# Kernel optimization log

Measured on AMD Instinct MI355X. Metric: run time of the kernel, lower is better.

Reference implementation:

```python
import jax, jax.numpy as jnp
import numpy as np

# Irrep layout: blocks of (multiplicity, l); identical for input and output.
LS = [0, 1, 2, 3]
MULS = [64, 64, 64, 64]
N = 65536
DIM = sum(m * (2 * l + 1) for m, l in zip(MULS, LS))  # 1024
NPATH = len(LS) * len(LS)  # 16 valid (l_out, l_in) paths
MAXM = max(LS)             # max |m| over all paths
NW = sum(mo * mi for mo in MULS for mi in MULS)  # 65536 path weights


def _split_blocks(x):
    """Split flat irrep vector into per-block [n, mul, 2l+1] views."""
    blocks, off = [], 0
    for mul, l in zip(MULS, LS):
        d = mul * (2 * l + 1)
        blocks.append(x[:, off:off + d].reshape(x.shape[0], mul, 2 * l + 1))
        off += d
    return blocks


def setup_inputs() -> dict:
    key = jax.random.key(0)
    k = jax.random.split(key, 5)
    return {
        "x": jax.random.normal(k[0], (N, DIM), jnp.float32),
        "weights": jax.random.normal(k[1], (NW,), jnp.float32) * 0.1,
        "hzero": jax.random.normal(k[2], (NPATH,), jnp.float32),
        "hpos": jax.random.normal(k[3], (NPATH, MAXM), jnp.float32),
        "hneg": jax.random.normal(k[4], (NPATH, MAXM), jnp.float32),
    }


def reference(x, weights, hzero, hpos, hneg):
    xb = _split_blocks(x)
    n = x.shape[0]
    outb = [jnp.zeros((n, mul, 2 * l + 1), x.dtype) for mul, l in zip(MULS, LS)]
    p, off = 0, 0
    for oi, (mo, lo) in enumerate(zip(MULS, LS)):
        for ii, (mi, li) in enumerate(zip(MULS, LS)):
            W = weights[off:off + mo * mi].reshape(mo, mi)
            off += mo * mi
            xi = xb[ii]  # [n, mi, 2*li+1]
            # m = 0 component
            y0 = jnp.einsum('nm,om->no', xi[:, :, li], W) * hzero[p]
            outb[oi] = outb[oi].at[:, :, lo].add(y0)
            # |m| >= 1: O(2)-reduced pos/neg mixing with Wigner-derived couplings
            for m in range(1, min(lo, li) + 1):
                hp, hn = hpos[p, m - 1], hneg[p, m - 1]
                xp, xn = xi[:, :, li + m], xi[:, :, li - m]
                outb[oi] = outb[oi].at[:, :, lo + m].add(
                    jnp.einsum('nm,om->no', hp * xp + hn * xn, W))
                outb[oi] = outb[oi].at[:, :, lo - m].add(
                    jnp.einsum('nm,om->no', hp * xn - hn * xp, W))
            p += 1
    return jnp.concatenate([b.reshape(n, -1) for b in outb], axis=1)
```

## Files before the change

### kernel.cpp

```cpp
#include <hip/hip_runtime.h>


typedef __attribute__((ext_vector_type(8))) short bhalf8_t;
typedef __attribute__((ext_vector_type(4))) float f32x4_t;

#define NROWS 65536
#define DIMV  1024
#define NT    1024
#define RPW   64

#define M0_OFF 0
#define M1_OFF 65536
#define M2_OFF 212992
#define M3_OFF 278528
#define M_TOTAL 294912

#define OP 1028

__device__ __forceinline__ constexpr int xoff(int L) {
    return (L == 0) ? 0 : (L == 1) ? 4608 : (L == 2) ? 18432 : 41472;
}

__device__ __forceinline__ short f2bf(float f) {
    unsigned u = __builtin_bit_cast(unsigned, f);
    u = (u + 0x7FFFu + ((u >> 16) & 1u)) >> 16;
    return (short)u;
}

__global__ __launch_bounds__(256) void build_M(const float* __restrict__ w,
                                               const float* __restrict__ hz,
                                               const float* __restrict__ hp,
                                               const float* __restrict__ hn,
                                               short* __restrict__ M) {
    int idx = blockIdx.x * 256 + threadIdx.x;
    if (idx >= M_TOTAL) return;

    int m, A, B;
    if (idx < M1_OFF)      { m = 0; int lo = idx;            A = lo / 256u; B = lo - A * 256; }
    else if (idx < M2_OFF) { m = 1; int lo = idx - M1_OFF;   A = lo / 384u; B = lo - A * 384; }
    else if (idx < M3_OFF) { m = 2; int lo = idx - M2_OFF;   A = lo / 256u; B = lo - A * 256; }
    else                   { m = 3; int lo = idx - M3_OFF;   A = lo / 128u; B = lo - A * 128; }

    int ob, so, o, ib, si, i;
    if (m == 0) { ob = A >> 6;       so = 0;            o = A & 63;
                  ib = B >> 6;       si = 0;            i = B & 63; }
    else        { ob = (A >> 7) + m; so = (A >> 6) & 1; o = A & 63;
                  ib = (B >> 7) + m; si = (B >> 6) & 1; i = B & 63; }

    int p = ob * 4 + ib;
    float wv = w[p * 4096 + o * 64 + i];
    float coef;
    if (m == 0) {
        coef = hz[p];
    } else {
        float hpv = hp[p * 3 + (m - 1)];
        float hnv = hn[p * 3 + (m - 1)];
        coef = (so == 0) ? ((si == 0) ? hpv : hnv)
                         : ((si == 0) ? -hnv : hpv);
    }
    M[idx] = f2bf(wv * coef);
}

template<int L>
__device__ __forceinline__ void stage_block(const float* __restrict__ x, int rowbase,
                                            short* __restrict__ xb, int tid) {
    constexpr int nch = 2 * L + 1;
    constexpr int d4  = 16 * nch;
    constexpr int RS  = nch * 72;
    constexpr int bo  = 64 * L * L;
#pragma unroll
    for (int e = 0; e < nch; ++e) {
        int id  = e * NT + tid;
        int row = id / d4;
        int cc  = id - row * d4;
        int col = cc * 4;
        const float4 v = *(const float4*)(x + (size_t)(rowbase + row) * DIMV + bo + col);
        short* dst = &xb[row * RS];
        { int ci = col;     int i = ci / nch; int ji = ci - i * nch; dst[ji * 72 + i] = f2bf(v.x); }
        { int ci = col + 1; int i = ci / nch; int ji = ci - i * nch; dst[ji * 72 + i] = f2bf(v.y); }
        { int ci = col + 2; int i = ci / nch; int ji = ci - i * nch; dst[ji * 72 + i] = f2bf(v.z); }
        { int ci = col + 3; int i = ci / nch; int ji = ci - i * nch; dst[ji * 72 + i] = f2bf(v.w); }
    }
}

template<int L>
__device__ __forceinline__ void compute_block(const short* __restrict__ xb,
                                              const short* __restrict__ Mg,
                                              int m, int Wm, int cb, int lr, int q,
                                              f32x4_t (&acc)[4][4]) {
    if (m > L) return;
    constexpr int nch = 2 * L + 1;
    constexpr int RS  = nch * 72;
    const int nsi = (m == 0) ? 1 : 2;
    for (int si = 0; si < nsi; ++si) {
        const int ji    = L + ((si == 0) ? m : -m);
        const int kbase = (m == 0) ? (L << 6) : (((L - m) << 7) + (si << 6));
#pragma unroll
        for (int kk = 0; kk < 2; ++kk) {
            bhalf8_t a[4];
            const int eo = ji * 72 + kk * 32 + q * 8;
#pragma unroll
            for (int r = 0; r < 4; ++r)
                a[r] = *(const bhalf8_t*)&xb[(r * 16 + lr) * RS + eo];
            const int ko = kbase + kk * 32 + q * 8;
#pragma unroll
            for (int c = 0; c < 4; ++c) {
                const bhalf8_t b = *(const bhalf8_t*)&Mg[(cb + c * 16 + lr) * Wm + ko];
#pragma unroll
                for (int r = 0; r < 4; ++r)
                    acc[c][r] = __builtin_amdgcn_mfma_f32_16x16x32_bf16(
                        a[r], b, acc[c][r], 0, 0, 0);
            }
        }
    }
}

__global__ __launch_bounds__(NT) void tp_main(const float* __restrict__ x,
                                              const short* __restrict__ Mall,
                                              float* __restrict__ out) {
    __shared__ __align__(16) char smem[147456];
    short* __restrict__ xbuf = (short*)smem;
    float* __restrict__ obuf = (float*)smem;

    const int tid  = threadIdx.x;
    const int lane = tid & 63;
    const int lr   = lane & 15;
    const int q    = lane >> 4;
    const int wv   = tid >> 6;
    const int rowbase = blockIdx.x * RPW;

    int m, cb;
    if (wv < 4)       { m = 0; cb = wv << 6; }
    else if (wv < 10) { m = 1; cb = (wv - 4) << 6; }
    else if (wv < 14) { m = 2; cb = (wv - 10) << 6; }
    else              { m = 3; cb = (wv - 14) << 6; }
    const int Wm   = (m == 1) ? 384 : ((m == 3) ? 128 : 256);
    const int Moff = (m == 0) ? M0_OFF : (m == 1) ? M1_OFF : (m == 2) ? M2_OFF : M3_OFF;
    const short* __restrict__ Mg = Mall + Moff;

    f32x4_t acc[4][4];
#pragma unroll
    for (int c = 0; c < 4; ++c)
#pragma unroll
        for (int r = 0; r < 4; ++r)
            acc[c][r] = (f32x4_t){0.f, 0.f, 0.f, 0.f};

    stage_block<0>(x, rowbase, xbuf + xoff(0), tid);
    stage_block<1>(x, rowbase, xbuf + xoff(1), tid);
    stage_block<2>(x, rowbase, xbuf + xoff(2), tid);
    stage_block<3>(x, rowbase, xbuf + xoff(3), tid);
    __syncthreads();

    compute_block<0>(xbuf + xoff(0), Mg, m, Wm, cb, lr, q, acc);
    compute_block<1>(xbuf + xoff(1), Mg, m, Wm, cb, lr, q, acc);
    compute_block<2>(xbuf + xoff(2), Mg, m, Wm, cb, lr, q, acc);
    compute_block<3>(xbuf + xoff(3), Mg, m, Wm, cb, lr, q, acc);

    int origc[4];
#pragma unroll
    for (int c = 0; c < 4; ++c) {
        const int P = cb + c * 16 + lr;
        int ob, o, jo;
        if (m == 0) { ob = P >> 6;       o = P & 63; jo = ob; }
        else        { ob = (P >> 7) + m; o = P & 63;
                      jo = ob + ((((P >> 6) & 1) == 0) ? m : -m); }
        origc[c] = 64 * ob * ob + o * (2 * ob + 1) + jo;
    }

#pragma unroll
    for (int r = 0; r < 4; ++r) {
        __syncthreads();
#pragma unroll
        for (int c = 0; c < 4; ++c) {
#pragma unroll
            for (int g = 0; g < 4; ++g)
                obuf[(q * 4 + g) * OP + origc[c]] = acc[c][r][g];
        }
        __syncthreads();
#pragma unroll
        for (int it = 0; it < 4; ++it) {
            const int j   = it * NT + tid;
            const int row = j >> 8;
            const int c4  = (j & 255) << 2;
            const float4 v = *(const float4*)&obuf[row * OP + c4];
            *(float4*)&out[(size_t)(rowbase + r * 16 + row) * DIMV + c4] = v;
        }
    }
}

extern "C" void kernel_launch(void* const* d_in, const int* in_sizes, int n_in,
                              void* d_out, int out_size, void* d_ws, size_t ws_size,
                              hipStream_t stream) {
    const float* x   = (const float*)d_in[0];
    const float* wts = (const float*)d_in[1];
    const float* hz  = (const float*)d_in[2];
    const float* hp  = (const float*)d_in[3];
    const float* hn  = (const float*)d_in[4];
    float* out = (float*)d_out;
    short* M   = (short*)d_ws;

    build_M<<<dim3(M_TOTAL / 256), dim3(256), 0, stream>>>(wts, hz, hp, hn, M);
    tp_main<<<dim3(NROWS / RPW), dim3(NT), 0, stream>>>(x, M, out);
}
```

Baseline: 528.7 us.

## Split x permutation into separate kernel and stream GEMM operands from global

Adds a pre-pass kernel that converts x to bf16 and writes it into per-m contiguous K-major segments in workspace. The main GEMM kernel then reads A and B fragments directly from global memory, with no LDS staging of x, and uses only a small LDS buffer for the output transpose, which should allow higher occupancy. A fallback kernel with reduced LDS, staging one L-block at a time, is used when the workspace is too small. The cost is an extra global round trip for the permuted bf16 x, about 128 MB written and read back.

```diff
diff --git a/kernel.cpp b/kernel.cpp
--- a/kernel.cpp
+++ b/kernel.cpp
@@ -6,8 +6,6 @@
 
 #define NROWS 65536
 #define DIMV  1024
-#define NT    1024
-#define RPW   64
 
 #define M0_OFF 0
 #define M1_OFF 65536
@@ -15,11 +13,14 @@
 #define M3_OFF 278528
 #define M_TOTAL 294912
 
+#define XG_SH_OFF 524288
+#define SEG0 0
+#define SEG1 16777216
+#define SEG2 41943040
+#define SEG3 58720256
+#define WS_NEED 135266304ull
+
 #define OP 1028
-
-__device__ __forceinline__ constexpr int xoff(int L) {
-    return (L == 0) ? 0 : (L == 1) ? 4608 : (L == 2) ? 18432 : 41472;
-}
 
 __device__ __forceinline__ short f2bf(float f) {
     unsigned u = __builtin_bit_cast(unsigned, f);
@@ -61,16 +62,145 @@
     M[idx] = f2bf(wv * coef);
 }
 
+__global__ __launch_bounds__(256) void permute_x(const float* __restrict__ x,
+                                                 short* __restrict__ xg) {
+    __shared__ __align__(16) short lbuf[16 * 1024];
+    const int t = threadIdx.x;
+    const int rowbase = blockIdx.x << 4;
+
+#pragma unroll
+    for (int p = 0; p < 16; ++p) {
+        const int id  = p * 256 + t;
+        const int row = id >> 8;
+        const int c4  = id & 255;
+        const float4 v = *(const float4*)(x + (size_t)(rowbase + row) * DIMV + c4 * 4);
+        short* d = &lbuf[row * 1024 + c4 * 4];
+        d[0] = f2bf(v.x); d[1] = f2bf(v.y); d[2] = f2bf(v.z); d[3] = f2bf(v.w);
+    }
+    __syncthreads();
+
+#pragma unroll
+    for (int p = 0; p < 8; ++p) {
+        const int cid = p * 256 + t;
+        const int row = cid >> 7;
+        const int kc  = cid & 127;
+        int m, klocal, Km; size_t seg;
+        if (kc < 32)       { m = 0; klocal = kc << 3;         Km = 256; seg = SEG0; }
+        else if (kc < 80)  { m = 1; klocal = (kc - 32) << 3;  Km = 384; seg = SEG1; }
+        else if (kc < 112) { m = 2; klocal = (kc - 80) << 3;  Km = 256; seg = SEG2; }
+        else               { m = 3; klocal = (kc - 112) << 3; Km = 128; seg = SEG3; }
+        int L, si, i0;
+        if (m == 0) { L = klocal >> 6;       si = 0;                 i0 = klocal & 63; }
+        else        { L = (klocal >> 7) + m; si = (klocal >> 6) & 1; i0 = klocal & 63; }
+        const int j    = (si == 0) ? (L + m) : (L - m);
+        const int st   = 2 * L + 1;
+        const int base = 64 * L * L + j + i0 * st;
+        const short* s = &lbuf[row * 1024];
+        bhalf8_t vv;
+#pragma unroll
+        for (int k = 0; k < 8; ++k) vv[k] = s[base + k * st];
+        *(bhalf8_t*)&xg[seg + (size_t)(rowbase + row) * Km + klocal] = vv;
+    }
+}
+
+__global__ __launch_bounds__(1024) void tp_gemm(const short* __restrict__ xg,
+                                                const short* __restrict__ Mall,
+                                                float* __restrict__ out) {
+    __shared__ __align__(16) float obuf[16 * OP];
+
+    const int tid  = threadIdx.x;
+    const int lane = tid & 63;
+    const int lr   = lane & 15;
+    const int q    = lane >> 4;
+    const int wv   = tid >> 6;
+    const int rowbase = blockIdx.x << 6;
+
+    int m, cb;
+    if (wv < 4)       { m = 0; cb = wv << 6; }
+    else if (wv < 10) { m = 1; cb = (wv - 4) << 6; }
+    else if (wv < 14) { m = 2; cb = (wv - 10) << 6; }
+    else              { m = 3; cb = (wv - 14) << 6; }
+    const int Wm   = (m == 1) ? 384 : ((m == 3) ? 128 : 256);
+    const int Moff = (m == 0) ? M0_OFF : (m == 1) ? M1_OFF : (m == 2) ? M2_OFF : M3_OFF;
+    const size_t xseg = (m == 0) ? SEG0 : (m == 1) ? SEG1 : (m == 2) ? SEG2 : SEG3;
+    const short* __restrict__ Mg  = Mall + Moff;
+    const short* __restrict__ xgm = xg + xseg;
+
+    const short* pa[4]; const short* pb[4];
+#pragma unroll
+    for (int r = 0; r < 4; ++r)
+        pa[r] = xgm + (size_t)(rowbase + r * 16 + lr) * Wm + q * 8;
+#pragma unroll
+    for (int c = 0; c < 4; ++c)
+        pb[c] = Mg + (size_t)(cb + c * 16 + lr) * Wm + q * 8;
+
+    f32x4_t acc[4][4];
+#pragma unroll
+    for (int c = 0; c < 4; ++c)
+#pragma unroll
+        for (int r = 0; r < 4; ++r)
+            acc[c][r] = (f32x4_t){0.f, 0.f, 0.f, 0.f};
+
+    const int nkc = Wm >> 5;
+#pragma unroll 2
+    for (int kc = 0; kc < nkc; ++kc) {
+        const int ko = kc * 32;
+        bhalf8_t a[4];
+#pragma unroll
+        for (int r = 0; r < 4; ++r)
+            a[r] = *(const bhalf8_t*)(pa[r] + ko);
+#pragma unroll
+        for (int c = 0; c < 4; ++c) {
+            const bhalf8_t b = *(const bhalf8_t*)(pb[c] + ko);
+#pragma unroll
+            for (int r = 0; r < 4; ++r)
+                acc[c][r] = __builtin_amdgcn_mfma_f32_16x16x32_bf16(
+                    a[r], b, acc[c][r], 0, 0, 0);
+        }
+    }
+
+    int origc[4];
+#pragma unroll
+    for (int c = 0; c < 4; ++c) {
+        const int P = cb + c * 16 + lr;
+        int ob, o, jo;
+        if (m == 0) { ob = P >> 6;       o = P & 63; jo = ob; }
+        else        { ob = (P >> 7) + m; o = P & 63;
+                      jo = ob + ((((P >> 6) & 1) == 0) ? m : -m); }
+        origc[c] = 64 * ob * ob + o * (2 * ob + 1) + jo;
+    }
+
+#pragma unroll
+    for (int r = 0; r < 4; ++r) {
+        if (r) __syncthreads();
+#pragma unroll
+        for (int c = 0; c < 4; ++c) {
+#pragma unroll
+            for (int g = 0; g < 4; ++g)
+                obuf[(q * 4 + g) * OP + origc[c]] = acc[c][r][g];
+        }
+        __syncthreads();
+#pragma unroll
+        for (int it = 0; it < 4; ++it) {
+            const int jj  = it * 1024 + tid;
+            const int row = jj >> 8;
+            const int c4  = (jj & 255) << 2;
+            const float4 v = *(const float4*)&obuf[row * OP + c4];
+            *(float4*)&out[(size_t)(rowbase + r * 16 + row) * DIMV + c4] = v;
+        }
+    }
+}
+
 template<int L>
-__device__ __forceinline__ void stage_block(const float* __restrict__ x, int rowbase,
-                                            short* __restrict__ xb, int tid) {
+__device__ __forceinline__ void stage_block_fb(const float* __restrict__ x, int rowbase,
+                                               short* __restrict__ xb, int tid) {
     constexpr int nch = 2 * L + 1;
     constexpr int d4  = 16 * nch;
     constexpr int RS  = nch * 72;
     constexpr int bo  = 64 * L * L;
 #pragma unroll
     for (int e = 0; e < nch; ++e) {
-        int id  = e * NT + tid;
+        int id  = e * 1024 + tid;
         int row = id / d4;
         int cc  = id - row * d4;
         int col = cc * 4;
@@ -84,10 +214,10 @@
 }
 
 template<int L>
-__device__ __forceinline__ void compute_block(const short* __restrict__ xb,
-                                              const short* __restrict__ Mg,
-                                              int m, int Wm, int cb, int lr, int q,
-                                              f32x4_t (&acc)[4][4]) {
+__device__ __forceinline__ void compute_block_fb(const short* __restrict__ xb,
+                                                 const short* __restrict__ Mg,
+                                                 int m, int Wm, int cb, int lr, int q,
+                                                 f32x4_t (&acc)[4][4]) {
     if (m > L) return;
     constexpr int nch = 2 * L + 1;
     constexpr int RS  = nch * 72;
@@ -115,10 +245,10 @@
     }
 }
 
-__global__ __launch_bounds__(NT) void tp_main(const float* __restrict__ x,
-                                              const short* __restrict__ Mall,
-                                              float* __restrict__ out) {
-    __shared__ __align__(16) char smem[147456];
+__global__ __launch_bounds__(1024) void tp_main_fb(const float* __restrict__ x,
+                                                   const short* __restrict__ Mall,
+                                                   float* __restrict__ out) {
+    __shared__ __align__(16) char smem[16 * OP * 4];
     short* __restrict__ xbuf = (short*)smem;
     float* __restrict__ obuf = (float*)smem;
 
@@ -127,7 +257,7 @@
     const int lr   = lane & 15;
     const int q    = lane >> 4;
     const int wv   = tid >> 6;
-    const int rowbase = blockIdx.x * RPW;
+    const int rowbase = blockIdx.x << 6;
 
     int m, cb;
     if (wv < 4)       { m = 0; cb = wv << 6; }
@@ -145,16 +275,22 @@
         for (int r = 0; r < 4; ++r)
             acc[c][r] = (f32x4_t){0.f, 0.f, 0.f, 0.f};
 
-    stage_block<0>(x, rowbase, xbuf + xoff(0), tid);
-    stage_block<1>(x, rowbase, xbuf + xoff(1), tid);
-    stage_block<2>(x, rowbase, xbuf + xoff(2), tid);
-    stage_block<3>(x, rowbase, xbuf + xoff(3), tid);
-    __syncthreads();
-
-    compute_block<0>(xbuf + xoff(0), Mg, m, Wm, cb, lr, q, acc);
-    compute_block<1>(xbuf + xoff(1), Mg, m, Wm, cb, lr, q, acc);
-    compute_block<2>(xbuf + xoff(2), Mg, m, Wm, cb, lr, q, acc);
-    compute_block<3>(xbuf + xoff(3), Mg, m, Wm, cb, lr, q, acc);
+    __syncthreads();
+    stage_block_fb<0>(x, rowbase, xbuf, tid);
+    __syncthreads();
+    compute_block_fb<0>(xbuf, Mg, m, Wm, cb, lr, q, acc);
+    __syncthreads();
+    stage_block_fb<1>(x, rowbase, xbuf, tid);
+    __syncthreads();
+    compute_block_fb<1>(xbuf, Mg, m, Wm, cb, lr, q, acc);
+    __syncthreads();
+    stage_block_fb<2>(x, rowbase, xbuf, tid);
+    __syncthreads();
+    compute_block_fb<2>(xbuf, Mg, m, Wm, cb, lr, q, acc);
+    __syncthreads();
+    stage_block_fb<3>(x, rowbase, xbuf, tid);
+    __syncthreads();
+    compute_block_fb<3>(xbuf, Mg, m, Wm, cb, lr, q, acc);
 
     int origc[4];
 #pragma unroll
@@ -179,9 +315,9 @@
         __syncthreads();
 #pragma unroll
         for (int it = 0; it < 4; ++it) {
-            const int j   = it * NT + tid;
-            const int row = j >> 8;
-            const int c4  = (j & 255) << 2;
+            const int jj  = it * 1024 + tid;
+            const int row = jj >> 8;
+            const int c4  = (jj & 255) << 2;
             const float4 v = *(const float4*)&obuf[row * OP + c4];
             *(float4*)&out[(size_t)(rowbase + r * 16 + row) * DIMV + c4] = v;
         }
@@ -198,7 +334,13 @@
     const float* hn  = (const float*)d_in[4];
     float* out = (float*)d_out;
     short* M   = (short*)d_ws;
+    short* xg  = (short*)d_ws + XG_SH_OFF;
 
     build_M<<<dim3(M_TOTAL / 256), dim3(256), 0, stream>>>(wts, hz, hp, hn, M);
-    tp_main<<<dim3(NROWS / RPW), dim3(NT), 0, stream>>>(x, M, out);
-}
+    if (ws_size >= WS_NEED) {
+        permute_x<<<dim3(NROWS / 16), dim3(256), 0, stream>>>(x, xg);
+        tp_gemm<<<dim3(NROWS / 64), dim3(1024), 0, stream>>>(xg, M, out);
+    } else {
+        tp_main_fb<<<dim3(NROWS / 64), dim3(1024), 0, stream>>>(x, M, out);
+    }
+}
```

Result: slower. 596.1 us (+12.8%).
